# Kernel tuning notes

Measured on AMD Instinct MI355X. Metric: run time of the kernel, lower is better.

Reference implementation:

```python
import jax, jax.numpy as jnp
import numpy as np

BETA = 50.0  # params['beta'] threshold for memory update
MEMORY_LEN = 4096


def setup_inputs() -> dict:
    key = jax.random.key(0)
    ks = jax.random.split(key, 7)
    B, D_IN, D_OUT, M = 256, 128, 256, MEMORY_LEN
    return {
        "x": jax.random.normal(ks[0], (B, D_IN), dtype=jnp.float32),
        "mean": jax.random.normal(ks[1], (D_IN,), dtype=jnp.float32),
        "std": jax.random.uniform(ks[2], (D_IN,), dtype=jnp.float32),
        "W1": jax.random.normal(ks[3], (D_IN, D_OUT), dtype=jnp.float32) * 0.1,
        "b1": jax.random.normal(ks[4], (D_OUT,), dtype=jnp.float32) * 0.1,
        "memory": jax.random.normal(ks[5], (M, D_OUT), dtype=jnp.float32),
        "mem_data": jax.random.normal(ks[6], (M, D_IN), dtype=jnp.float32),
    }


def reference(x, mean, std, W1, b1, memory, mem_data):
    # normalize, zeroing columns where std == 0 (as in torch forward)
    zero_std = std == 0
    denom = jnp.where(zero_std, 1.0, std)
    new = jnp.where(zero_std[None, :], 0.0, (x - mean) / denom)  # [B, D_in]

    # encoder: Linear + Tanh
    enc = jnp.tanh(new @ W1 + b1)  # [B, D_out]

    # L1 cdist against full memory (count == memory_len, steady state) + row min
    dist = jnp.abs(enc[:, None, :] - memory[None, :, :]).sum(-1)  # [B, M]
    loss = dist.min(axis=1)  # [B]

    # sequential per-row circular-buffer scatter update (side effect in torch)
    M = memory.shape[0]

    def step(carry, inp):
        mem, md, count = carry
        l, e, xi = inp
        cond = jnp.isfinite(l) & (l <= BETA)
        pos = jnp.mod(count, M)
        mem = mem.at[pos].set(jnp.where(cond, e, mem[pos]))
        md = md.at[pos].set(jnp.where(cond, xi, md[pos]))
        return (mem, md, count + cond.astype(jnp.int32)), None

    # count starts at memory_len (memory full), so writes wrap from position 0
    (mem_out, md_out, _), _ = jax.lax.scan(
        step, (memory, mem_data, jnp.int32(M)), (loss, enc, x)
    )
    return loss, mem_out, md_out
```

## Files before the change

kernel.cpp:

```cpp
#include <hip/hip_runtime.h>
#include <hip/hip_bf16.h>
#include <math.h>

#define B_ROWS 256
#define D_IN   128
#define D_OUT  256
#define M_LEN  4096
#define BETA   50.0f

#define OFF_MEM  (B_ROWS)
#define OFF_MD   (B_ROWS + M_LEN * D_OUT)

__global__ __launch_bounds__(256) void k_prep(
    const float* __restrict__ x, const float* __restrict__ mean,
    const float* __restrict__ stdv, const float* __restrict__ W1,
    const float* __restrict__ b1, float* __restrict__ enc,
    float* __restrict__ out) {
  __shared__ float sx[D_IN];
  const int b = blockIdx.x, j = threadIdx.x;
  if (j < D_IN) {
    float s = stdv[j];
    sx[j] = (s == 0.0f) ? 0.0f : (x[b * D_IN + j] - mean[j]) / s;
  }
  __syncthreads();
  float acc = b1[j];
#pragma unroll 8
  for (int k = 0; k < D_IN; ++k) acc = fmaf(sx[k], W1[k * D_OUT + j], acc);
  enc[b * D_OUT + j] = tanhf(acc);
  if (b == 0) ((unsigned int*)out)[j] = 0x7F800000u;
}

#define TB 32
#define TM 64

__global__ __launch_bounds__(256) void k_dist(
    const float* __restrict__ enc, const float* __restrict__ mem,
    const float4* __restrict__ mem4, const float4* __restrict__ md4,
    float* __restrict__ out) {
  __shared__ __align__(16) float sE[4][32][TB];
  __shared__ __align__(16) float sM[4][32][TM];

  const int t  = threadIdx.x;
  const int w  = t >> 6;
  const int l  = t & 63;
  const int ro = l >> 3;
  const int q  = l & 7;
  const int m0 = blockIdx.x * TM;
  const int b0 = blockIdx.y * TB;
  const int bid = blockIdx.y * 64 + blockIdx.x;

  const float* encp = enc + (b0 + ro) * D_OUT + w * 64 + q * 4;
  const float* memp = mem + (m0 + ro) * D_OUT + w * 64 + q * 4;

  float4 rE[4], rM[8], rE2[4], rM2[8];
  float acc[4][8] = {};

  auto store_lds = [&](const float4* e, const float4* m) {
#pragma unroll
    for (int i = 0; i < 4; ++i) {
      const int row = (i * 8 + ro) ^ (q * 4);
      sE[w][q * 4 + 0][row] = e[i].x;
      sE[w][q * 4 + 1][row] = e[i].y;
      sE[w][q * 4 + 2][row] = e[i].z;
      sE[w][q * 4 + 3][row] = e[i].w;
    }
#pragma unroll
    for (int i = 0; i < 8; ++i) {
      const int row = (i * 8 + ro) ^ (q * 4);
      sM[w][q * 4 + 0][row] = m[i].x;
      sM[w][q * 4 + 1][row] = m[i].y;
      sM[w][q * 4 + 2][row] = m[i].z;
      sM[w][q * 4 + 3][row] = m[i].w;
    }
  };

  auto rdE = [&](int kk) -> float4 {
    const int sw = (kk >> 2) * 4;
    return *(const float4*)&sE[w][kk][(ro * 4) ^ sw];
  };
  auto rdM1 = [&](int kk) -> float4 {
    const int sw = (kk >> 2) * 4;
    return *(const float4*)&sM[w][kk][(q * 8) ^ sw];
  };
  auto rdM2 = [&](int kk) -> float4 {
    const int sw = (kk >> 2) * 4;
    return *(const float4*)&sM[w][kk][(q * 8 + 4) ^ sw];
  };

  auto compute = [&]() {
    __builtin_amdgcn_s_setprio(1);
    float4 bE[4], bM1[4], bM2[4];
#pragma unroll
    for (int p = 0; p < 4; ++p) {
      bE[p] = rdE(p); bM1[p] = rdM1(p); bM2[p] = rdM2(p);
    }
#pragma unroll
    for (int kk = 0; kk < 32; ++kk) {
      const int s = kk & 3;
      float4 a  = bE[s];
      float4 v1 = bM1[s];
      float4 v2 = bM2[s];
      if (kk + 4 < 32) {
        bE[s] = rdE(kk + 4); bM1[s] = rdM1(kk + 4); bM2[s] = rdM2(kk + 4);
      }
      float av[4] = {a.x, a.y, a.z, a.w};
      float bw[8] = {v1.x, v1.y, v1.z, v1.w, v2.x, v2.y, v2.z, v2.w};
#pragma unroll
      for (int i = 0; i < 4; ++i)
#pragma unroll
        for (int j = 0; j < 8; ++j) {
          float d = av[i] - bw[j];
          asm("v_add_f32 %0, %0, |%1|" : "+v"(acc[i][j]) : "v"(d));
        }
    }
    __builtin_amdgcn_s_setprio(0);
  };

#pragma unroll
  for (int i = 0; i < 4; ++i) rE[i] = *(const float4*)(encp + i * 8 * D_OUT);
#pragma unroll
  for (int i = 0; i < 8; ++i) rM[i] = *(const float4*)(memp + i * 8 * D_OUT);
  store_lds(rE, rM);

#pragma unroll
  for (int i = 0; i < 4; ++i) rE2[i] = *(const float4*)(encp + 32 + i * 8 * D_OUT);
#pragma unroll
  for (int i = 0; i < 8; ++i) rM2[i] = *(const float4*)(memp + 32 + i * 8 * D_OUT);

  float4 cm0 = mem4[bid * 512 + t];
  float4 cm1 = mem4[bid * 512 + 256 + t];
  float4 cd0 = md4[bid * 256 + t];

  compute();
  store_lds(rE2, rM2);
  compute();

  float* sf = &sM[0][0][0];
#pragma unroll
  for (int i = 0; i < 4; ++i)
#pragma unroll
    for (int j = 0; j < 8; ++j) {
      const int p = i * 8 + j;
      sf[w * 2048 + l * 32 + (p ^ (l & 31))] = acc[i][j];
    }
  __syncthreads();

  {
    const int r = t >> 3, cg = t & 7;
    const int lv = (r >> 2) * 8 + cg;
    float dmin = 3.4e38f;
#pragma unroll
    for (int j = 0; j < 8; ++j) {
      const int p = (r & 3) * 8 + j;
      float s = sf[0 * 2048 + lv * 32 + (p ^ (lv & 31))];
      s += sf[1 * 2048 + lv * 32 + (p ^ (lv & 31))];
      s += sf[2 * 2048 + lv * 32 + (p ^ (lv & 31))];
      s += sf[3 * 2048 + lv * 32 + (p ^ (lv & 31))];
      dmin = fminf(dmin, s);
    }
    dmin = fminf(dmin, __shfl_xor(dmin, 1));
    dmin = fminf(dmin, __shfl_xor(dmin, 2));
    dmin = fminf(dmin, __shfl_xor(dmin, 4));
    if (cg == 0)
      atomicMin((unsigned int*)out + (b0 + r), __float_as_uint(dmin));
  }

  float4* mo = (float4*)(out + OFF_MEM);
  float4* dd = (float4*)(out + OFF_MD);
  mo[bid * 512 + t] = cm0;
  mo[bid * 512 + 256 + t] = cm1;
  dd[bid * 256 + t] = cd0;
}

__global__ __launch_bounds__(256) void k_scatter(float* __restrict__ out,
                                                 const float* __restrict__ enc,
                                                 const float* __restrict__ x) {
  __shared__ int wcount[4];
  int t = threadIdx.x;
  float l = out[t];
  bool cond = isfinite(l) && (l <= BETA);
  unsigned long long m = __ballot(cond);
  int lane = t & 63;
  int wv   = t >> 6;
  int pre_in_wave = __popcll(m & ((1ull << lane) - 1ull));
  if (lane == 0) wcount[wv] = (int)__popcll(m);
  __syncthreads();
  int base = 0;
  for (int w = 0; w < wv; ++w) base += wcount[w];
  if (cond) {
    int pos = base + pre_in_wave;
    float* mrow = out + OFF_MEM + pos * D_OUT;
    const float* erow = enc + t * D_OUT;
    for (int d = 0; d < D_OUT; ++d) mrow[d] = erow[d];
    float* drow = out + OFF_MD + pos * D_IN;
    const float* xrow = x + t * D_IN;
    for (int d = 0; d < D_IN; ++d) drow[d] = xrow[d];
  }
}

extern "C" void kernel_launch(void* const* d_in, const int* in_sizes, int n_in,
                              void* d_out, int out_size, void* d_ws, size_t ws_size,
                              hipStream_t stream) {
  const float* x      = (const float*)d_in[0];
  const float* mean   = (const float*)d_in[1];
  const float* stdv   = (const float*)d_in[2];
  const float* W1     = (const float*)d_in[3];
  const float* b1     = (const float*)d_in[4];
  const float* memory = (const float*)d_in[5];
  const float* memdat = (const float*)d_in[6];
  float* out = (float*)d_out;
  float* enc = (float*)d_ws;

  k_prep<<<dim3(B_ROWS), dim3(256), 0, stream>>>(x, mean, stdv, W1, b1, enc, out);

  k_dist<<<dim3(M_LEN / TM, B_ROWS / TB), dim3(256), 0, stream>>>(
      enc, memory, (const float4*)memory, (const float4*)memdat, out);

  k_scatter<<<dim3(1), dim3(256), 0, stream>>>(out, enc, x);
}
```

Measured before the change: 26.53 us.

## Compute L1 distances in packed fp16 with half2 LDS tiles

Converts the encoder and memory tiles to fp16 when staging them in shared memory. The abs-difference accumulation then runs as packed half2 subtract, abs and add, processing two feature dimensions per instruction. This roughly halves the ALU work and the LDS footprint of the distance loop, and the per-lane accumulators are widened back to float before the cross-wave reduction. The cost is accuracy: fp16 rounding of inputs and fp16 accumulation of partial sums of up to 32 terms can shift the row minimum and flip the beta threshold decision.

```diff
diff --git a/kernel.cpp b/kernel.cpp
--- a/kernel.cpp
+++ b/kernel.cpp
@@ -1,5 +1,6 @@
 #include <hip/hip_runtime.h>
 #include <hip/hip_bf16.h>
+#include <hip/hip_fp16.h>
 #include <math.h>
 
 #define B_ROWS 256
@@ -10,6 +11,8 @@
 
 #define OFF_MEM  (B_ROWS)
 #define OFF_MD   (B_ROWS + M_LEN * D_OUT)
+
+#define H2(f) __builtin_bit_cast(__half2, f)
 
 __global__ __launch_bounds__(256) void k_prep(
     const float* __restrict__ x, const float* __restrict__ mean,
@@ -37,8 +40,8 @@
     const float* __restrict__ enc, const float* __restrict__ mem,
     const float4* __restrict__ mem4, const float4* __restrict__ md4,
     float* __restrict__ out) {
-  __shared__ __align__(16) float sE[4][32][TB];
-  __shared__ __align__(16) float sM[4][32][TM];
+  __shared__ __align__(16) float sf[8192];
+  __half2* sh = reinterpret_cast<__half2*>(sf);
 
   const int t  = threadIdx.x;
   const int w  = t >> 6;
@@ -52,39 +55,49 @@
   const float* encp = enc + (b0 + ro) * D_OUT + w * 64 + q * 4;
   const float* memp = mem + (m0 + ro) * D_OUT + w * 64 + q * 4;
 
+  const int web = w * 2048;
+  const int wmb = w * 2048 + 512;
+  const int lk  = q;
+
   float4 rE[4], rM[8], rE2[4], rM2[8];
-  float acc[4][8] = {};
+  __half2 acc_h[4][8];
+#pragma unroll
+  for (int i = 0; i < 4; ++i)
+#pragma unroll
+    for (int j = 0; j < 8; ++j) acc_h[i][j] = __float2half2_rn(0.0f);
 
   auto store_lds = [&](const float4* e, const float4* m) {
+    const int eb0 = web + (2 * lk) * 32;
+    const int mb0 = wmb + (2 * lk) * 64;
 #pragma unroll
     for (int i = 0; i < 4; ++i) {
-      const int row = (i * 8 + ro) ^ (q * 4);
-      sE[w][q * 4 + 0][row] = e[i].x;
-      sE[w][q * 4 + 1][row] = e[i].y;
-      sE[w][q * 4 + 2][row] = e[i].z;
-      sE[w][q * 4 + 3][row] = e[i].w;
+      __half2 h0 = __float22half2_rn(make_float2(e[i].x, e[i].y));
+      __half2 h1 = __float22half2_rn(make_float2(e[i].z, e[i].w));
+      const int rp = (ro + 8 * i) ^ (4 * lk);
+      sh[eb0 + rp] = h0;
+      sh[eb0 + 32 + rp] = h1;
     }
 #pragma unroll
     for (int i = 0; i < 8; ++i) {
-      const int row = (i * 8 + ro) ^ (q * 4);
-      sM[w][q * 4 + 0][row] = m[i].x;
-      sM[w][q * 4 + 1][row] = m[i].y;
-      sM[w][q * 4 + 2][row] = m[i].z;
-      sM[w][q * 4 + 3][row] = m[i].w;
-    }
-  };
-
-  auto rdE = [&](int kk) -> float4 {
-    const int sw = (kk >> 2) * 4;
-    return *(const float4*)&sE[w][kk][(ro * 4) ^ sw];
-  };
-  auto rdM1 = [&](int kk) -> float4 {
-    const int sw = (kk >> 2) * 4;
-    return *(const float4*)&sM[w][kk][(q * 8) ^ sw];
-  };
-  auto rdM2 = [&](int kk) -> float4 {
-    const int sw = (kk >> 2) * 4;
-    return *(const float4*)&sM[w][kk][(q * 8 + 4) ^ sw];
+      __half2 g0 = __float22half2_rn(make_float2(m[i].x, m[i].y));
+      __half2 g1 = __float22half2_rn(make_float2(m[i].z, m[i].w));
+      const int cp = (ro + 8 * i) ^ (8 * (lk & 3));
+      sh[mb0 + cp] = g0;
+      sh[mb0 + 64 + cp] = g1;
+    }
+  };
+
+  auto rdE = [&](int kk2) -> float4 {
+    const int u = (kk2 >> 1) & 7;
+    return *(const float4*)&sh[web + kk2 * 32 + ((4 * ro) ^ (4 * u))];
+  };
+  auto rdM1 = [&](int kk2) -> float4 {
+    const int u = (kk2 >> 1) & 3;
+    return *(const float4*)&sh[wmb + kk2 * 64 + ((8 * q) ^ (8 * u))];
+  };
+  auto rdM2 = [&](int kk2) -> float4 {
+    const int u = (kk2 >> 1) & 3;
+    return *(const float4*)&sh[wmb + kk2 * 64 + ((8 * q) ^ (8 * u)) + 4];
   };
 
   auto compute = [&]() {
@@ -95,22 +108,25 @@
       bE[p] = rdE(p); bM1[p] = rdM1(p); bM2[p] = rdM2(p);
     }
 #pragma unroll
-    for (int kk = 0; kk < 32; ++kk) {
-      const int s = kk & 3;
+    for (int kk2 = 0; kk2 < 16; ++kk2) {
+      const int s = kk2 & 3;
       float4 a  = bE[s];
       float4 v1 = bM1[s];
       float4 v2 = bM2[s];
-      if (kk + 4 < 32) {
-        bE[s] = rdE(kk + 4); bM1[s] = rdM1(kk + 4); bM2[s] = rdM2(kk + 4);
+      if (kk2 + 4 < 16) {
+        bE[s] = rdE(kk2 + 4); bM1[s] = rdM1(kk2 + 4); bM2[s] = rdM2(kk2 + 4);
       }
-      float av[4] = {a.x, a.y, a.z, a.w};
-      float bw[8] = {v1.x, v1.y, v1.z, v1.w, v2.x, v2.y, v2.z, v2.w};
+      __half2 av[4]  = {H2(a.x), H2(a.y), H2(a.z), H2(a.w)};
+      __half2 b1h[4] = {H2(v1.x), H2(v1.y), H2(v1.z), H2(v1.w)};
+      __half2 b2h[4] = {H2(v2.x), H2(v2.y), H2(v2.z), H2(v2.w)};
 #pragma unroll
       for (int i = 0; i < 4; ++i)
 #pragma unroll
-        for (int j = 0; j < 8; ++j) {
-          float d = av[i] - bw[j];
-          asm("v_add_f32 %0, %0, |%1|" : "+v"(acc[i][j]) : "v"(d));
+        for (int j = 0; j < 4; ++j) {
+          acc_h[i][j]     = __hadd2(acc_h[i][j],
+                                    __habs2(__hsub2(av[i], b1h[j])));
+          acc_h[i][j + 4] = __hadd2(acc_h[i][j + 4],
+                                    __habs2(__hsub2(av[i], b2h[j])));
         }
     }
     __builtin_amdgcn_s_setprio(0);
@@ -135,13 +151,13 @@
   store_lds(rE2, rM2);
   compute();
 
-  float* sf = &sM[0][0][0];
 #pragma unroll
   for (int i = 0; i < 4; ++i)
 #pragma unroll
     for (int j = 0; j < 8; ++j) {
+      float2 pr = __half22float2(acc_h[i][j]);
       const int p = i * 8 + j;
-      sf[w * 2048 + l * 32 + (p ^ (l & 31))] = acc[i][j];
+      sf[w * 2048 + l * 32 + (p ^ (l & 31))] = pr.x + pr.y;
     }
   __syncthreads();
 
```

Result: slower. 29.56 us (+11.4%).
